# Optimization experiments

Hardware: AMD Instinct MI355X
Metric: run time of the kernel (lower is better)

## Reference

```python
import jax, jax.numpy as jnp
import numpy as np

H = W = 32      # latent grid
WS = 8          # window size
NH = 8          # heads
C = 512         # channels
SHIFTS = (0, WS // 2)  # depth-2 Swin stage: W-MSA then SW-MSA


def _rel_pos_index(ws):
    coords = np.stack(np.meshgrid(np.arange(ws), np.arange(ws), indexing='ij'))
    flat = coords.reshape(2, -1)
    rel = (flat[:, :, None] - flat[:, None, :]).transpose(1, 2, 0).copy()
    rel[:, :, 0] += ws - 1
    rel[:, :, 1] += ws - 1
    rel[:, :, 0] *= 2 * ws - 1
    return jnp.asarray(rel.sum(-1))  # (ws*ws, ws*ws) int


def _attn_mask(h, w, ws, shift):
    img = np.zeros((h, w))
    cnt = 0
    sl = (slice(0, -ws), slice(-ws, -shift), slice(-shift, None))
    for hs in sl:
        for wsl in sl:
            img[hs, wsl] = cnt
            cnt += 1
    mw = img.reshape(h // ws, ws, w // ws, ws).transpose(0, 2, 1, 3).reshape(-1, ws * ws)
    m = mw[:, None, :] - mw[:, :, None]  # matches unsqueeze(1) - unsqueeze(2)
    return jnp.asarray(np.where(m != 0, -100.0, 0.0).astype(np.float32))  # (nW, N, N)


def _ln(x, g, b, eps=1e-5):
    mu = x.mean(-1, keepdims=True)
    var = ((x - mu) ** 2).mean(-1, keepdims=True)
    return (x - mu) * jax.lax.rsqrt(var + eps) * g + b


def _swin_block(x, shift, mask, rpi, n1g, n1b, qw, qb, rpb, pw, pb, n2g, n2b, f1w, f1b, f2w, f2b):
    B, L, Cc = x.shape
    N = WS * WS
    hd = Cc // NH
    shortcut = x
    h = _ln(x, n1g, n1b).reshape(B, H, W, Cc)
    if shift > 0:
        h = jnp.roll(h, (-shift, -shift), (1, 2))
    # window partition -> (B*nW, N, C)
    hw = h.reshape(B, H // WS, WS, W // WS, WS, Cc).transpose(0, 1, 3, 2, 4, 5).reshape(-1, N, Cc)
    qkv = (hw @ qw + qb).reshape(-1, N, 3, NH, hd).transpose(2, 0, 3, 1, 4)
    q, k, v = qkv[0], qkv[1], qkv[2]
    attn = jnp.einsum('bhnd,bhmd->bhnm', q * (hd ** -0.5), k)
    bias = rpb[rpi.reshape(-1)].reshape(N, N, NH).transpose(2, 0, 1)  # (NH, N, N)
    attn = attn + bias[None]
    if mask is not None:
        nW = mask.shape[0]
        attn = attn.reshape(-1, nW, NH, N, N) + mask[None, :, None]
        attn = attn.reshape(-1, NH, N, N)
    attn = jax.nn.softmax(attn, axis=-1)
    o = jnp.einsum('bhnm,bhmd->bhnd', attn, v).transpose(0, 2, 1, 3).reshape(-1, N, Cc)
    o = o @ pw + pb
    # window reverse
    o = o.reshape(B, H // WS, W // WS, WS, WS, Cc).transpose(0, 1, 3, 2, 4, 5).reshape(B, H, W, Cc)
    if shift > 0:
        o = jnp.roll(o, (shift, shift), (1, 2))
    x = shortcut + o.reshape(B, L, Cc)
    h2 = _ln(x, n2g, n2b)
    x = x + (jax.nn.gelu(h2 @ f1w + f1b, approximate=False) @ f2w + f2b)
    return x


def setup_inputs() -> dict:
    key = jax.random.key(0)
    ks = jax.random.split(key, 8)
    B, D, K = 32, 2, 4096
    s = 0.02
    return {
        'x': jax.random.normal(ks[0], (B, H * W, C), jnp.float32),
        'norm1_g': jnp.ones((D, C), jnp.float32),
        'norm1_b': jnp.zeros((D, C), jnp.float32),
        'qkv_w': jax.random.normal(ks[1], (D, C, 3 * C), jnp.float32) * s,
        'qkv_b': jnp.zeros((D, 3 * C), jnp.float32),
        'rpb_table': jax.random.normal(ks[2], (D, (2 * WS - 1) ** 2, NH), jnp.float32) * s,
        'proj_w': jax.random.normal(ks[3], (D, C, C), jnp.float32) * s,
        'proj_b': jnp.zeros((D, C), jnp.float32),
        'norm2_g': jnp.ones((D, C), jnp.float32),
        'norm2_b': jnp.zeros((D, C), jnp.float32),
        'fc1_w': jax.random.normal(ks[4], (D, C, 4 * C), jnp.float32) * s,
        'fc1_b': jnp.zeros((D, 4 * C), jnp.float32),
        'fc2_w': jax.random.normal(ks[5], (D, 4 * C, C), jnp.float32) * s,
        'fc2_b': jnp.zeros((D, C), jnp.float32),
        'codebook': jax.random.normal(ks[6], (K, C), jnp.float32),
    }


def reference(x, norm1_g, norm1_b, qkv_w, qkv_b, rpb_table, proj_w, proj_b,
              norm2_g, norm2_b, fc1_w, fc1_b, fc2_w, fc2_b, codebook):
    B, L, Cc = x.shape
    rpi = _rel_pos_index(WS)
    masks = [None, _attn_mask(H, W, WS, SHIFTS[1])]
    for i, shift in enumerate(SHIFTS):
        x = _swin_block(x, shift, masks[i], rpi,
                        norm1_g[i], norm1_b[i], qkv_w[i], qkv_b[i], rpb_table[i],
                        proj_w[i], proj_b[i], norm2_g[i], norm2_b[i],
                        fc1_w[i], fc1_b[i], fc2_w[i], fc2_b[i])
    # nearest-neighbor codebook quantization (cdist + argmin + gather)
    flat = x.reshape(-1, Cc)
    d = ((flat ** 2).sum(-1, keepdims=True)
         - 2.0 * flat @ codebook.T
         + (codebook ** 2).sum(-1))  # (B*L, K)
    idx = jnp.argmin(d, axis=-1)
    quant = codebook[idx]
    # straight-through estimator
    quant = flat + jax.lax.stop_gradient(quant - flat)
    return quant.reshape(B, L, Cc), idx.reshape(B, L)
```

## Files before the change

kernel.cpp:

```cpp
#include <hip/hip_runtime.h>
#include <math.h>

#define DEV __device__ __forceinline__

typedef __attribute__((ext_vector_type(8))) _Float16 f16x8;
typedef __attribute__((ext_vector_type(8))) short short8;
typedef __attribute__((ext_vector_type(4))) float f32x4;

namespace {

constexpr int C = 512;
constexpr int ROWS = 32768;
constexpr float LSCALE = 2048.0f;
constexpr float LINV   = 1.0f / 2048.0f;
constexpr float F16MIN = 6.1035156e-5f;

DEV void f2hsplit(float x, short& hs, short& ls) {
  _Float16 h = (_Float16)x;
  float hf = (float)h;
  if (fabsf(hf) < F16MIN) { h = (_Float16)0.0f; hf = 0.f; }
  _Float16 l = (_Float16)((x - hf) * LSCALE);
  if (fabsf((float)l) < F16MIN) l = (_Float16)0.0f;
  hs = __builtin_bit_cast(short, h);
  ls = __builtin_bit_cast(short, l);
}

DEV unsigned umn(unsigned a, unsigned b) { return a < b ? a : b; }
DEV unsigned umx(unsigned a, unsigned b) { return a > b ? a : b; }

DEV unsigned packkey(float d, int col) {
  unsigned u = __builtin_bit_cast(unsigned, d);
  u = (u & 0x80000000u) ? ~u : (u | 0x80000000u);
  return (u & 0xFFFFF000u) | (unsigned)col;
}
DEV float unpackd(unsigned k) {
  unsigned u = (k & 0x80000000u) ? (k ^ 0x80000000u) : ~k;
  return __builtin_bit_cast(float, u);
}

DEV int rowmap(int r, int shift) {
  int b  = r >> 10;
  int w  = (r >> 6) & 15;
  int wy = w >> 2, wx = w & 3;
  int ii = r & 63;
  int iy = ii >> 3, ix = ii & 7;
  int y = (wy * 8 + iy + shift) & 31;
  int x = (wx * 8 + ix + shift) & 31;
  return (b << 10) + (y << 5) + x;
}

DEV int region(int y) { return (y < 24) ? 0 : ((y < 28) ? 1 : 2); }

typedef __attribute__((address_space(1))) const unsigned int gu32;
typedef __attribute__((address_space(3))) unsigned int lu32;
DEV void gload16(const void* g, void* l) {
  __builtin_amdgcn_global_load_lds((gu32*)g, (lu32*)l, 16, 0, 0);
}

__global__ __launch_bounds__(256) void ln_split_kernel(
    const float* __restrict__ src, short* __restrict__ Hp, short* __restrict__ Lp,
    const float* __restrict__ g, const float* __restrict__ b,
    int shift, int windowed) {
  int wid  = (blockIdx.x * 256 + threadIdx.x) >> 6;
  int lane = threadIdx.x & 63;
  if (wid >= ROWS) return;
  int srcRow = windowed ? rowmap(wid, shift) : wid;
  const float* s = src + (size_t)srcRow * C + lane * 8;
  float v[8];
  *(float4*)(v)     = *(const float4*)(s);
  *(float4*)(v + 4) = *(const float4*)(s + 4);
  float sum = 0.f;
#pragma unroll
  for (int j = 0; j < 8; j++) sum += v[j];
#pragma unroll
  for (int o = 32; o >= 1; o >>= 1) sum += __shfl_xor(sum, o);
  float mu = sum * (1.0f / 512.0f);
  float vs = 0.f;
#pragma unroll
  for (int j = 0; j < 8; j++) { float d = v[j] - mu; vs += d * d; }
#pragma unroll
  for (int o = 32; o >= 1; o >>= 1) vs += __shfl_xor(vs, o);
  float rs = rsqrtf(vs * (1.0f / 512.0f) + 1e-5f);
  float gg[8], bb[8];
  *(float4*)gg       = *(const float4*)&g[lane * 8];
  *(float4*)(gg + 4) = *(const float4*)&g[lane * 8 + 4];
  *(float4*)bb       = *(const float4*)&b[lane * 8];
  *(float4*)(bb + 4) = *(const float4*)&b[lane * 8 + 4];
  short8 hv, lv;
#pragma unroll
  for (int j = 0; j < 8; j++) {
    float o8 = (v[j] - mu) * rs * gg[j] + bb[j];
    short hh, ll;
    f2hsplit(o8, hh, ll);
    hv[j] = hh; lv[j] = ll;
  }
  *(short8*)&Hp[(size_t)wid * C + lane * 8] = hv;
  *(short8*)&Lp[(size_t)wid * C + lane * 8] = lv;
}

__global__ __launch_bounds__(256) void rowss_kernel(
    const float* __restrict__ src, float* __restrict__ dst, int nrows) {
  int wid  = (blockIdx.x * 256 + threadIdx.x) >> 6;
  int lane = threadIdx.x & 63;
  if (wid >= nrows) return;
  const float* s = src + (size_t)wid * C + lane * 8;
  float4 a  = *(const float4*)s;
  float4 b4 = *(const float4*)(s + 4);
  float sum = a.x*a.x + a.y*a.y + a.z*a.z + a.w*a.w
            + b4.x*b4.x + b4.y*b4.y + b4.z*b4.z + b4.w*b4.w;
#pragma unroll
  for (int o = 32; o >= 1; o >>= 1) sum += __shfl_xor(sum, o);
  if (lane == 0) dst[wid] = sum;
}

__global__ __launch_bounds__(256) void wconvT_kernel(
    const float* __restrict__ W, short* __restrict__ Hp, short* __restrict__ Lp,
    int K, int N) {
  __shared__ float t[32][33];
  int tx = threadIdx.x, ty = threadIdx.y;
  int n0 = blockIdx.x * 32, k0 = blockIdx.y * 32;
#pragma unroll
  for (int r = 0; r < 4; r++) {
    int k = ty + r * 8;
    t[k][tx] = W[(size_t)(k0 + k) * N + n0 + tx];
  }
  __syncthreads();
#pragma unroll
  for (int r = 0; r < 4; r++) {
    int n = ty + r * 8;
    short h, l;
    f2hsplit(t[tx][n], h, l);
    Hp[(size_t)(n0 + n) * K + k0 + tx] = h;
    Lp[(size_t)(n0 + n) * K + k0 + tx] = l;
  }
}

__global__ __launch_bounds__(256) void wconv_kernel(
    const float* __restrict__ W, short* __restrict__ Hp, short* __restrict__ Lp) {
  size_t i = ((size_t)blockIdx.x * 256 + threadIdx.x) * 4;
  float4 a = *(const float4*)&W[i];
  float v[4] = {a.x, a.y, a.z, a.w};
  short hv[4], lv[4];
#pragma unroll
  for (int j = 0; j < 4; j++) f2hsplit(v[j], hv[j], lv[j]);
  *(short4*)&Hp[i] = *(short4*)hv;
  *(short4*)&Lp[i] = *(short4*)lv;
}

template <int EPI>
__global__ __launch_bounds__(512) void mgemm(
    const short* __restrict__ Ah, const short* __restrict__ Al,
    const short* __restrict__ Bh, const short* __restrict__ Bl,
    const int K, const float* __restrict__ bias,
    float* __restrict__ outF, short* __restrict__ outH, short* __restrict__ outL,
    const int ldo,
    const float* __restrict__ resid, const int rowOff, const int perm, const int shift) {
  __shared__ short lds[32768];
  const int m0 = blockIdx.x * 128, n0 = blockIdx.y * 128;
  const int t  = threadIdx.x;
  const int wv = t >> 6, ln = t & 63;
  const int wr = (wv >> 2) * 64, wc = (wv & 3) * 32;
  const int l15 = ln & 15, l4 = ln >> 4;

  f32x4 accH[4][2], accL[4][2];
#pragma unroll
  for (int mf = 0; mf < 4; mf++)
#pragma unroll
    for (int nf = 0; nf < 2; nf++) {
      accH[mf][nf] = (f32x4){0.f, 0.f, 0.f, 0.f};
      accL[mf][nf] = (f32x4){0.f, 0.f, 0.f, 0.f};
    }

  const int srow = ln >> 2;
  const int scol = ((ln & 3) ^ ((ln >> 3) & 3)) * 8;

  auto stage = [&](int buf, int k0) {
    short* b = lds + buf * 16384;
    size_t ra = (size_t)(m0 + wv * 16 + srow) * K + k0 + scol;
    size_t rb = (size_t)(n0 + wv * 16 + srow) * K + k0 + scol;
    gload16(Ah + ra, b + wv * 512);
    gload16(Bh + rb, b + 4096 + wv * 512);
    gload16(Al + ra, b + 8192 + wv * 512);
    gload16(Bl + rb, b + 12288 + wv * 512);
  };
  auto frag = [&](const short* lt, int rbase) -> f16x8 {
    int r = rbase + l15;
    int kc = l4 ^ ((r >> 1) & 3);
    return *(const f16x8*)(lt + (r >> 4) * 512 + (r & 15) * 32 + kc * 8);
  };

  stage(0, 0);
  __syncthreads();
  int cur = 0;
  for (int k0 = 0; k0 < K; k0 += 32) {
    if (k0 + 32 < K) stage(cur ^ 1, k0 + 32);
    const short* base = lds + cur * 16384;
    const short* As_h = base;
    const short* Bs_h = base + 4096;
    const short* As_l = base + 8192;
    const short* Bs_l = base + 12288;
    f16x8 ah[4], bh[2], bl[2];
#pragma unroll
    for (int mf = 0; mf < 4; mf++) ah[mf] = frag(As_h, wr + mf * 16);
#pragma unroll
    for (int nf = 0; nf < 2; nf++) bh[nf] = frag(Bs_h, wc + nf * 16);
#pragma unroll
    for (int mf = 0; mf < 4; mf++)
#pragma unroll
      for (int nf = 0; nf < 2; nf++)
        accH[mf][nf] = __builtin_amdgcn_mfma_f32_16x16x32_f16(ah[mf], bh[nf], accH[mf][nf], 0, 0, 0);
#pragma unroll
    for (int nf = 0; nf < 2; nf++) bl[nf] = frag(Bs_l, wc + nf * 16);
#pragma unroll
    for (int mf = 0; mf < 4; mf++)
#pragma unroll
      for (int nf = 0; nf < 2; nf++)
        accL[mf][nf] = __builtin_amdgcn_mfma_f32_16x16x32_f16(ah[mf], bl[nf], accL[mf][nf], 0, 0, 0);
#pragma unroll
    for (int mf = 0; mf < 4; mf++) {
      f16x8 al = frag(As_l, wr + mf * 16);
#pragma unroll
      for (int nf = 0; nf < 2; nf++)
        accL[mf][nf] = __builtin_amdgcn_mfma_f32_16x16x32_f16(al, bh[nf], accL[mf][nf], 0, 0, 0);
    }
    __syncthreads();
    cur ^= 1;
  }

  f32x4 acc[4][2];
#pragma unroll
  for (int mf = 0; mf < 4; mf++)
#pragma unroll
    for (int nf = 0; nf < 2; nf++)
#pragma unroll
      for (int r = 0; r < 4; r++)
        acc[mf][nf][r] = fmaf(accL[mf][nf][r], LINV, accH[mf][nf][r]);

  if (EPI == 0) {
#pragma unroll
    for (int mf = 0; mf < 4; mf++)
#pragma unroll
      for (int r = 0; r < 4; r++) {
        int row = m0 + wr + mf * 16 + l4 * 4 + r;
        float* op = outF + (size_t)row * ldo;
#pragma unroll
        for (int nf = 0; nf < 2; nf++) {
          int col = n0 + wc + nf * 16 + l15;
          op[col] = acc[mf][nf][r] + bias[col];
        }
      }
  } else if (EPI == 1) {
#pragma unroll
    for (int mf = 0; mf < 4; mf++)
#pragma unroll
      for (int r = 0; r < 4; r++) {
        int row = m0 + wr + mf * 16 + l4 * 4 + r;
#pragma unroll
        for (int nf = 0; nf < 2; nf++) {
          int col = n0 + wc + nf * 16 + l15;
          float v = acc[mf][nf][r] + bias[col];
          v = 0.5f * v * (1.0f + erff(v * 0.70710678118654752f));
          short h, l;
          f2hsplit(v, h, l);
          outH[(size_t)row * ldo + col] = h;
          outL[(size_t)row * ldo + col] = l;
        }
      }
  } else {
#pragma unroll
    for (int mf = 0; mf < 4; mf++)
#pragma unroll
      for (int r = 0; r < 4; r++) {
        int row = m0 + wr + mf * 16 + l4 * 4 + r;
        int orow = perm ? rowmap(row, shift) : (row + rowOff);
        const float* rp = resid + (size_t)orow * ldo;
        float* op = outF + (size_t)orow * ldo;
#pragma unroll
        for (int nf = 0; nf < 2; nf++) {
          int col = n0 + wc + nf * 16 + l15;
          float v = rp[col] + acc[mf][nf][r] + bias[col];
          op[col] = v;
          if (EPI == 4) {
            short h, l;
            f2hsplit(v, h, l);
            outH[(size_t)orow * ldo + col] = h;
            outL[(size_t)orow * ldo + col] = l;
          }
        }
      }
  }
}

__global__ __launch_bounds__(512) void vqgemm(
    const short* __restrict__ Ah, const short* __restrict__ Bh,
    const float* __restrict__ c2, unsigned* __restrict__ pk) {
  __shared__ short lds[12288];
  const int bid = blockIdx.x;
  const int xcd = bid & 7, idx = bid >> 3;
  const int m0 = (xcd * 32 + (idx & 31)) * 128;
  const int ny = idx >> 5;
  const int n0 = ny * 256;
  const int K = 512;
  const int t  = threadIdx.x;
  const int wv = t >> 6, ln = t & 63;
  const int wr = (wv >> 2) * 64, wc = (wv & 3) * 64;
  const int l15 = ln & 15, l4 = ln >> 4;

  f32x4 acc[4][4];
#pragma unroll
  for (int mf = 0; mf < 4; mf++)
#pragma unroll
    for (int nf = 0; nf < 4; nf++) acc[mf][nf] = (f32x4){0.f, 0.f, 0.f, 0.f};

  const int srow = ln >> 2;
  const int scol = ((ln & 3) ^ ((ln >> 3) & 3)) * 8;

  short* As = lds;
  short* Bs = lds + 4096;

  auto frag = [&](const short* lt, int rbase) -> f16x8 {
    int r = rbase + l15;
    int kc = l4 ^ ((r >> 1) & 3);
    return *(const f16x8*)(lt + (r >> 4) * 512 + (r & 15) * 32 + kc * 8);
  };

  for (int k0 = 0; k0 < K; k0 += 32) {
#pragma unroll
    for (int q = 0; q < 3; q++) {
      int s = wv * 3 + q;
      int isA = (s < 8);
      int c = isA ? s : (s - 8);
      const short* src = isA ? Ah : Bh;
      short* dst = (isA ? As : Bs) + c * 512;
      int rowbase = (isA ? m0 : n0) + c * 16;
      size_t ga = (size_t)(rowbase + srow) * K + k0 + scol;
      gload16(src + ga, dst);
    }
    __syncthreads();
    f16x8 ah[4], bh[4];
#pragma unroll
    for (int mf = 0; mf < 4; mf++) ah[mf] = frag(As, wr + mf * 16);
#pragma unroll
    for (int nf = 0; nf < 4; nf++) bh[nf] = frag(Bs, wc + nf * 16);
#pragma unroll
    for (int mf = 0; mf < 4; mf++)
#pragma unroll
      for (int nf = 0; nf < 4; nf++)
        acc[mf][nf] = __builtin_amdgcn_mfma_f32_16x16x32_f16(ah[mf], bh[nf], acc[mf][nf], 0, 0, 0);
    __syncthreads();
  }

  unsigned* hk = (unsigned*)(void*)lds;
#pragma unroll
  for (int mf = 0; mf < 4; mf++)
#pragma unroll
    for (int r = 0; r < 4; r++) {
      int wrow = wr + mf * 16 + l4 * 4 + r;
      unsigned k1 = 0xFFFFFFFFu, k2 = 0xFFFFFFFFu;
#pragma unroll
      for (int nf = 0; nf < 4; nf++) {
        int col = n0 + wc + nf * 16 + l15;
        float d = c2[col] - 2.0f * acc[mf][nf][r];
        unsigned kk = packkey(d, col);
        if (kk < k1) { k2 = k1; k1 = kk; }
        else if (kk < k2) { k2 = kk; }
      }
#pragma unroll
      for (int o = 1; o <= 8; o <<= 1) {
        unsigned b1 = (unsigned)__shfl_xor((int)k1, o);
        unsigned b2 = (unsigned)__shfl_xor((int)k2, o);
        unsigned m1 = umn(k1, b1);
        unsigned m2 = umn(umx(k1, b1), umn(k2, b2));
        k1 = m1; k2 = m2;
      }
      if (l15 == 0) {
        hk[wrow * 8 + (wv & 3) * 2 + 0] = k1;
        hk[wrow * 8 + (wv & 3) * 2 + 1] = k2;
      }
    }
  __syncthreads();
  if (t < 128) {
    unsigned q1[4], q2[4];
#pragma unroll
    for (int i = 0; i < 4; i++) {
      q1[i] = hk[t * 8 + i * 2];
      q2[i] = hk[t * 8 + i * 2 + 1];
    }
    unsigned a1 = umn(q1[0], q1[1]);
    unsigned a2 = umn(umx(q1[0], q1[1]), umn(q2[0], q2[1]));
    unsigned b1 = umn(q1[2], q1[3]);
    unsigned b2 = umn(umx(q1[2], q1[3]), umn(q2[2], q2[3]));
    unsigned m1 = umn(a1, b1);
    unsigned m2 = umn(umx(a1, b1), umn(a2, b2));
    size_t base = (size_t)(m0 + t) * 32 + ny * 2;
    pk[base + 0] = m1;
    pk[base + 1] = m2;
  }
}

__global__ __launch_bounds__(256) void vq_out_kernel(
    const unsigned* __restrict__ pk, const float* __restrict__ x,
    const float* __restrict__ cb,
    float* __restrict__ outq, float* __restrict__ outidx) {
  int r = blockIdx.x * 4 + (threadIdx.x >> 6);
  int lane = threadIdx.x & 63;
  unsigned key = (lane < 32) ? pk[(size_t)r * 32 + lane] : 0xFFFFFFFFu;
  unsigned kmin = key;
#pragma unroll
  for (int o = 32; o >= 1; o >>= 1) kmin = umn(kmin, (unsigned)__shfl_xor((int)kmin, o));
  float dmin = unpackd(kmin);
  unsigned long long mask = __ballot(lane < 32 && unpackd(key) <= dmin + 2.0f);

  const float* xr = x + (size_t)r * C + lane * 8;
  float4 xa = *(const float4*)xr;
  float4 xb = *(const float4*)(xr + 4);

  float bestd = 3.4e38f;
  int   besti = 0x7fffffff;
  while (mask) {
    int l = __ffsll(mask) - 1;
    mask &= mask - 1;
    int col = ((unsigned)__shfl((int)key, l)) & 0xFFFu;
    const float* cr = cb + (size_t)col * C + lane * 8;
    float4 ca = *(const float4*)cr;
    float4 cb4 = *(const float4*)(cr + 4);
    float s = 0.f;
    s = fmaf(ca.x, ca.x - 2.f * xa.x, s);
    s = fmaf(ca.y, ca.y - 2.f * xa.y, s);
    s = fmaf(ca.z, ca.z - 2.f * xa.z, s);
    s = fmaf(ca.w, ca.w - 2.f * xa.w, s);
    s = fmaf(cb4.x, cb4.x - 2.f * xb.x, s);
    s = fmaf(cb4.y, cb4.y - 2.f * xb.y, s);
    s = fmaf(cb4.z, cb4.z - 2.f * xb.z, s);
    s = fmaf(cb4.w, cb4.w - 2.f * xb.w, s);
#pragma unroll
    for (int o = 32; o >= 1; o >>= 1) s += __shfl_xor(s, o);
    if (s < bestd || (s == bestd && col < besti)) { bestd = s; besti = col; }
  }
  const float4* src = (const float4*)(cb + (size_t)besti * C + lane * 8);
  float4*       dst = (float4*)(outq + (size_t)r * C + lane * 8);
  dst[0] = src[0];
  dst[1] = src[1];
  if (lane == 0) outidx[r] = (float)besti;
}

__global__ __launch_bounds__(256) void attn_kernel(
    const float* __restrict__ qkv,
    const float* __restrict__ rpb,
    short* __restrict__ Hout, short* __restrict__ Lout,
    int winOff, int shift) {
  int wl = blockIdx.x;
  int h  = blockIdx.y;
  int t  = threadIdx.x;
  __shared__ float q[64][64], k[64][64], v[64][64], pT[64][64];

  const float* base = qkv + (size_t)wl * 64 * 1536 + h * 64;
#pragma unroll
  for (int rep = 0; rep < 4; rep++) {
    int f = t + rep * 256;
    int i = f >> 4, dq = (f & 15) * 4;
    const float* rowp = base + (size_t)i * 1536 + dq;
    float4 qv = *(const float4*)(rowp);
    float4 kv = *(const float4*)(rowp + 512);
    float4 vv = *(const float4*)(rowp + 1024);
    q[i][dq] = qv.x * 0.125f; q[i][dq + 1] = qv.y * 0.125f;
    q[i][dq + 2] = qv.z * 0.125f; q[i][dq + 3] = qv.w * 0.125f;
    *(float4*)&k[i][dq] = kv;
    *(float4*)&v[i][dq] = vv;
  }
  __syncthreads();

  int i  = t >> 2;
  int jg = t & 3;
  int wim = (winOff + wl) & 15;
  int wy = wim >> 2, wx = wim & 3;
  int iy = i >> 3, ix = i & 7;

  float qreg[64];
#pragma unroll
  for (int d = 0; d < 64; d += 4) *(float4*)&qreg[d] = *(float4*)&q[i][d];

  int ci = 0;
  if (shift) ci = region(wy * 8 + iy) * 3 + region(wx * 8 + ix);

  float sc[16];
#pragma unroll
  for (int jj = 0; jj < 16; jj++) {
    int j = jg * 16 + jj;
    float s = 0.f;
#pragma unroll
    for (int d = 0; d < 64; d += 4) {
      float4 kv = *(float4*)&k[j][d];
      s = fmaf(qreg[d], kv.x, s);
      s = fmaf(qreg[d + 1], kv.y, s);
      s = fmaf(qreg[d + 2], kv.z, s);
      s = fmaf(qreg[d + 3], kv.w, s);
    }
    int jy = j >> 3, jx = j & 7;
    s += rpb[((iy - jy + 7) * 15 + (ix - jx + 7)) * 8 + h];
    if (shift) {
      int cj = region(wy * 8 + jy) * 3 + region(wx * 8 + jx);
      if (ci != cj) s -= 100.0f;
    }
    sc[jj] = s;
  }
  float mx = sc[0];
#pragma unroll
  for (int jj = 1; jj < 16; jj++) mx = fmaxf(mx, sc[jj]);
  mx = fmaxf(mx, __shfl_xor(mx, 1));
  mx = fmaxf(mx, __shfl_xor(mx, 2));
  float sum = 0.f;
#pragma unroll
  for (int jj = 0; jj < 16; jj++) { sc[jj] = expf(sc[jj] - mx); sum += sc[jj]; }
  sum += __shfl_xor(sum, 1);
  sum += __shfl_xor(sum, 2);
  float inv = 1.0f / sum;
#pragma unroll
  for (int jj = 0; jj < 16; jj++) pT[jg * 16 + jj][i] = sc[jj] * inv;
  __syncthreads();

  float accv[16];
#pragma unroll
  for (int dd = 0; dd < 16; dd++) accv[dd] = 0.f;
  for (int j = 0; j < 64; j++) {
    float pij = pT[j][i];
#pragma unroll
    for (int dd = 0; dd < 16; dd += 4) {
      float4 vv = *(float4*)&v[j][jg * 16 + dd];
      accv[dd]     = fmaf(pij, vv.x, accv[dd]);
      accv[dd + 1] = fmaf(pij, vv.y, accv[dd + 1]);
      accv[dd + 2] = fmaf(pij, vv.z, accv[dd + 2]);
      accv[dd + 3] = fmaf(pij, vv.w, accv[dd + 3]);
    }
  }
  size_t obase = ((size_t)(winOff + wl) * 64 + i) * 512 + h * 64 + jg * 16;
  short8 hv, lv;
#pragma unroll
  for (int half = 0; half < 2; half++) {
#pragma unroll
    for (int j = 0; j < 8; j++) {
      short hh, ll;
      f2hsplit(accv[half * 8 + j], hh, ll);
      hv[j] = hh; lv[j] = ll;
    }
    *(short8*)&Hout[obase + half * 8] = hv;
    *(short8*)&Lout[obase + half * 8] = lv;
  }
}

}

extern "C" void kernel_launch(void* const* d_in, const int* in_sizes, int n_in,
                              void* d_out, int out_size, void* d_ws, size_t ws_size,
                              hipStream_t stream) {
  const float* x_in = (const float*)d_in[0];
  const float* n1g  = (const float*)d_in[1];
  const float* n1b  = (const float*)d_in[2];
  const float* qkvw = (const float*)d_in[3];
  const float* qkvb = (const float*)d_in[4];
  const float* rpb  = (const float*)d_in[5];
  const float* pw   = (const float*)d_in[6];
  const float* pb   = (const float*)d_in[7];
  const float* n2g  = (const float*)d_in[8];
  const float* n2b  = (const float*)d_in[9];
  const float* f1w  = (const float*)d_in[10];
  const float* f1b  = (const float*)d_in[11];
  const float* f2w  = (const float*)d_in[12];
  const float* f2b_ = (const float*)d_in[13];
  const float* cb   = (const float*)d_in[14];

  float* outq   = (float*)d_out;
  float* outidx = outq + 16777216;
  short* Hbuf = (short*)d_out;
  short* Lbuf = Hbuf + (size_t)ROWS * 512;

  char* ws = (char*)d_ws;
  float* Abuf = (float*)ws;
  short* Wb   = (short*)(ws + ((size_t)64 << 20));
  char*  Cbuf = ws + ((size_t)96 << 20);
  const int Rrows = (ws_size >= ((size_t)232 << 20)) ? 16384
                  : (ws_size >= ((size_t)160 << 20)) ? 8192
                  : (ws_size >= ((size_t)128 << 20)) ? 4096 : 2048;

  const int SZ_QKV = 512 * 1536, SZ_P = 512 * 512, SZ_F1 = 512 * 2048, SZ_F2 = 2048 * 512;
  const int PB = (SZ_QKV + SZ_P + SZ_F1 + SZ_F2) * 2;
  short* cbH = Wb + (size_t)2 * PB;
  short* cbL = cbH + 4096 * 512;

  for (int blk = 0; blk < 2; blk++) {
    short* base = Wb + (size_t)blk * PB;
    short* qH = base;          short* qL = qH + SZ_QKV;
    short* pH = qL + SZ_QKV;   short* pL = pH + SZ_P;
    short* f1H = pL + SZ_P;    short* f1L = f1H + SZ_F1;
    short* f2H = f1L + SZ_F1;  short* f2L = f2H + SZ_F2;
    wconvT_kernel<<<dim3(48, 16), dim3(32, 8), 0, stream>>>(qkvw + (size_t)blk * SZ_QKV, qH, qL, 512, 1536);
    wconvT_kernel<<<dim3(16, 16), dim3(32, 8), 0, stream>>>(pw + (size_t)blk * SZ_P, pH, pL, 512, 512);
    wconvT_kernel<<<dim3(64, 16), dim3(32, 8), 0, stream>>>(f1w + (size_t)blk * SZ_F1, f1H, f1L, 512, 2048);
    wconvT_kernel<<<dim3(16, 64), dim3(32, 8), 0, stream>>>(f2w + (size_t)blk * SZ_F2, f2H, f2L, 2048, 512);
  }
  wconv_kernel<<<2048, 256, 0, stream>>>(cb, cbH, cbL);

  const int nch = ROWS / Rrows;
  for (int blk = 0; blk < 2; blk++) {
    short* base = Wb + (size_t)blk * PB;
    short* qH = base;          short* qL = qH + SZ_QKV;
    short* pH = qL + SZ_QKV;   short* pL = pH + SZ_P;
    short* f1H = pL + SZ_P;    short* f1L = f1H + SZ_F1;
    short* f2H = f1L + SZ_F1;  short* f2L = f2H + SZ_F2;
    const float* xcur = blk ? (const float*)Abuf : x_in;
    int shift = blk ? 4 : 0;

    ln_split_kernel<<<8192, 256, 0, stream>>>(xcur, Hbuf, Lbuf, n1g + blk * 512, n1b + blk * 512, shift, 1);

    float* Cq = (float*)Cbuf;
    for (int ch = 0; ch < nch; ch++) {
      int r0 = ch * Rrows;
      mgemm<0><<<dim3(Rrows / 128, 12), 512, 0, stream>>>(
          Hbuf + (size_t)r0 * 512, Lbuf + (size_t)r0 * 512, qH, qL, 512,
          qkvb + blk * 1536, Cq, nullptr, nullptr, 1536,
          nullptr, 0, 0, 0);
      attn_kernel<<<dim3(Rrows / 64, 8), 256, 0, stream>>>(
          Cq, rpb + blk * 1800, Hbuf, Lbuf, r0 >> 6, shift);
    }

    mgemm<2><<<dim3(256, 4), 512, 0, stream>>>(
        Hbuf, Lbuf, pH, pL, 512, pb + blk * 512,
        Abuf, nullptr, nullptr, 512,
        blk ? (const float*)Abuf : x_in, 0, 1, shift);

    ln_split_kernel<<<8192, 256, 0, stream>>>(Abuf, Hbuf, Lbuf, n2g + blk * 512, n2b + blk * 512, 0, 0);

    short* gh = (short*)Cbuf;
    short* gl = gh + (size_t)Rrows * 2048;
    for (int ch = 0; ch < nch; ch++) {
      int r0 = ch * Rrows;
      mgemm<1><<<dim3(Rrows / 128, 16), 512, 0, stream>>>(
          Hbuf + (size_t)r0 * 512, Lbuf + (size_t)r0 * 512, f1H, f1L, 512,
          f1b + blk * 2048, nullptr, gh, gl, 2048,
          nullptr, 0, 0, 0);
      if (blk == 0) {
        mgemm<2><<<dim3(Rrows / 128, 4), 512, 0, stream>>>(
            gh, gl, f2H, f2L, 2048, f2b_ + blk * 512,
            Abuf, nullptr, nullptr, 512,
            Abuf, r0, 0, 0);
      } else {
        mgemm<4><<<dim3(Rrows / 128, 4), 512, 0, stream>>>(
            gh, gl, f2H, f2L, 2048, f2b_ + blk * 512,
            Abuf, Hbuf, Lbuf, 512,
            Abuf, r0, 0, 0);
      }
    }
  }

  float*    c2  = (float*)Cbuf;
  unsigned* pkb = (unsigned*)(Cbuf + ((size_t)64 << 10));
  rowss_kernel<<<1024, 256, 0, stream>>>(cb, c2, 4096);
  vqgemm<<<4096, 512, 0, stream>>>(Hbuf, cbH, c2, pkb);
  vq_out_kernel<<<8192, 256, 0, stream>>>(pkb, Abuf, cb, outq, outidx);
}
```

Before: 2.331 ms.

## Widen split-fp16 GEMM tiles to 128x256 and double-buffer the VQ GEMM

Adds a wgemm kernel with 128x256 output tiles (16 accumulator fragments per wave for each of the high and low parts) and uses it for the QKV, attention projection and FC1 GEMMs, which halves the grid in N. This raises operand reuse per LDS load but roughly doubles accumulator registers and LDS (96KB), which may reduce occupancy. The VQ distance GEMM gains a double-buffered LDS staging pipeline so the next K-tile loads while the current one runs on MFMA. The mgemm kernel is trimmed to only its residual epilogues.

After: 2.724 ms. 16.8% more time.

```diff
diff --git a/kernel.cpp b/kernel.cpp
--- a/kernel.cpp
+++ b/kernel.cpp
@@ -145,6 +145,143 @@
   for (int j = 0; j < 4; j++) f2hsplit(v[j], hv[j], lv[j]);
   *(short4*)&Hp[i] = *(short4*)hv;
   *(short4*)&Lp[i] = *(short4*)lv;
+}
+
+template <int EPI>
+__global__ __launch_bounds__(512) void wgemm(
+    const short* __restrict__ Ah, const short* __restrict__ Al,
+    const short* __restrict__ Bh, const short* __restrict__ Bl,
+    const int K, const float* __restrict__ bias,
+    float* __restrict__ outF, short* __restrict__ outH, short* __restrict__ outL,
+    const int ldo,
+    const float* __restrict__ resid, const int rowOff, const int perm, const int shift) {
+  __shared__ short lds[49152];
+  const int m0 = blockIdx.x * 128, n0 = blockIdx.y * 256;
+  const int t  = threadIdx.x;
+  const int wv = t >> 6, ln = t & 63;
+  const int wr = (wv >> 2) * 64, wc = (wv & 3) * 64;
+  const int l15 = ln & 15, l4 = ln >> 4;
+
+  f32x4 accH[4][4], accL[4][4];
+#pragma unroll
+  for (int mf = 0; mf < 4; mf++)
+#pragma unroll
+    for (int nf = 0; nf < 4; nf++) {
+      accH[mf][nf] = (f32x4){0.f, 0.f, 0.f, 0.f};
+      accL[mf][nf] = (f32x4){0.f, 0.f, 0.f, 0.f};
+    }
+
+  const int srow = ln >> 2;
+  const int scol = ((ln & 3) ^ ((ln >> 3) & 3)) * 8;
+
+  auto stage = [&](int buf, int k0) {
+    short* b = lds + buf * 24576;
+#pragma unroll
+    for (int q = 0; q < 6; q++) {
+      int s = wv * 6 + q;
+      const short* src; short* dstp; int rowbase;
+      if (s < 8)       { src = Ah; dstp = b + s * 512;                rowbase = m0 + s * 16; }
+      else if (s < 24) { src = Bh; dstp = b + 4096 + (s - 8) * 512;   rowbase = n0 + (s - 8) * 16; }
+      else if (s < 32) { src = Al; dstp = b + 12288 + (s - 24) * 512; rowbase = m0 + (s - 24) * 16; }
+      else             { src = Bl; dstp = b + 16384 + (s - 32) * 512; rowbase = n0 + (s - 32) * 16; }
+      gload16(src + (size_t)(rowbase + srow) * K + k0 + scol, dstp);
+    }
+  };
+  auto frag = [&](const short* lt, int rbase) -> f16x8 {
+    int r = rbase + l15;
+    int kc = l4 ^ ((r >> 1) & 3);
+    return *(const f16x8*)(lt + (r >> 4) * 512 + (r & 15) * 32 + kc * 8);
+  };
+
+  stage(0, 0);
+  __syncthreads();
+  int cur = 0;
+  for (int k0 = 0; k0 < K; k0 += 32) {
+    if (k0 + 32 < K) stage(cur ^ 1, k0 + 32);
+    const short* b = lds + cur * 24576;
+    f16x8 ah[4], bh[4], bl[4];
+#pragma unroll
+    for (int mf = 0; mf < 4; mf++) ah[mf] = frag(b, wr + mf * 16);
+#pragma unroll
+    for (int nf = 0; nf < 4; nf++) bh[nf] = frag(b + 4096, wc + nf * 16);
+#pragma unroll
+    for (int mf = 0; mf < 4; mf++)
+#pragma unroll
+      for (int nf = 0; nf < 4; nf++)
+        accH[mf][nf] = __builtin_amdgcn_mfma_f32_16x16x32_f16(ah[mf], bh[nf], accH[mf][nf], 0, 0, 0);
+#pragma unroll
+    for (int nf = 0; nf < 4; nf++) bl[nf] = frag(b + 16384, wc + nf * 16);
+#pragma unroll
+    for (int mf = 0; mf < 4; mf++)
+#pragma unroll
+      for (int nf = 0; nf < 4; nf++)
+        accL[mf][nf] = __builtin_amdgcn_mfma_f32_16x16x32_f16(ah[mf], bl[nf], accL[mf][nf], 0, 0, 0);
+#pragma unroll
+    for (int mf = 0; mf < 4; mf++) {
+      f16x8 al = frag(b + 12288, wr + mf * 16);
+#pragma unroll
+      for (int nf = 0; nf < 4; nf++)
+        accL[mf][nf] = __builtin_amdgcn_mfma_f32_16x16x32_f16(al, bh[nf], accL[mf][nf], 0, 0, 0);
+    }
+    __syncthreads();
+    cur ^= 1;
+  }
+
+  f32x4 acc[4][4];
+#pragma unroll
+  for (int mf = 0; mf < 4; mf++)
+#pragma unroll
+    for (int nf = 0; nf < 4; nf++)
+#pragma unroll
+      for (int r = 0; r < 4; r++)
+        acc[mf][nf][r] = fmaf(accL[mf][nf][r], LINV, accH[mf][nf][r]);
+
+  if (EPI == 0) {
+#pragma unroll
+    for (int mf = 0; mf < 4; mf++)
+#pragma unroll
+      for (int r = 0; r < 4; r++) {
+        int row = m0 + wr + mf * 16 + l4 * 4 + r;
+        float* op = outF + (size_t)row * ldo;
+#pragma unroll
+        for (int nf = 0; nf < 4; nf++) {
+          int col = n0 + wc + nf * 16 + l15;
+          op[col] = acc[mf][nf][r] + bias[col];
+        }
+      }
+  } else if (EPI == 1) {
+#pragma unroll
+    for (int mf = 0; mf < 4; mf++)
+#pragma unroll
+      for (int r = 0; r < 4; r++) {
+        int row = m0 + wr + mf * 16 + l4 * 4 + r;
+#pragma unroll
+        for (int nf = 0; nf < 4; nf++) {
+          int col = n0 + wc + nf * 16 + l15;
+          float v = acc[mf][nf][r] + bias[col];
+          v = 0.5f * v * (1.0f + erff(v * 0.70710678118654752f));
+          short h, l;
+          f2hsplit(v, h, l);
+          outH[(size_t)row * ldo + col] = h;
+          outL[(size_t)row * ldo + col] = l;
+        }
+      }
+  } else {
+#pragma unroll
+    for (int mf = 0; mf < 4; mf++)
+#pragma unroll
+      for (int r = 0; r < 4; r++) {
+        int row = m0 + wr + mf * 16 + l4 * 4 + r;
+        int orow = perm ? rowmap(row, shift) : (row + rowOff);
+        const float* rp = resid + (size_t)orow * ldo;
+        float* op = outF + (size_t)orow * ldo;
+#pragma unroll
+        for (int nf = 0; nf < 4; nf++) {
+          int col = n0 + wc + nf * 16 + l15;
+          op[col] = rp[col] + acc[mf][nf][r] + bias[col];
+        }
+      }
+  }
 }
 
 template <int EPI>
@@ -195,22 +332,18 @@
   for (int k0 = 0; k0 < K; k0 += 32) {
     if (k0 + 32 < K) stage(cur ^ 1, k0 + 32);
     const short* base = lds + cur * 16384;
-    const short* As_h = base;
-    const short* Bs_h = base + 4096;
-    const short* As_l = base + 8192;
-    const short* Bs_l = base + 12288;
     f16x8 ah[4], bh[2], bl[2];
 #pragma unroll
-    for (int mf = 0; mf < 4; mf++) ah[mf] = frag(As_h, wr + mf * 16);
-#pragma unroll
-    for (int nf = 0; nf < 2; nf++) bh[nf] = frag(Bs_h, wc + nf * 16);
+    for (int mf = 0; mf < 4; mf++) ah[mf] = frag(base, wr + mf * 16);
+#pragma unroll
+    for (int nf = 0; nf < 2; nf++) bh[nf] = frag(base + 4096, wc + nf * 16);
 #pragma unroll
     for (int mf = 0; mf < 4; mf++)
 #pragma unroll
       for (int nf = 0; nf < 2; nf++)
         accH[mf][nf] = __builtin_amdgcn_mfma_f32_16x16x32_f16(ah[mf], bh[nf], accH[mf][nf], 0, 0, 0);
 #pragma unroll
-    for (int nf = 0; nf < 2; nf++) bl[nf] = frag(Bs_l, wc + nf * 16);
+    for (int nf = 0; nf < 2; nf++) bl[nf] = frag(base + 12288, wc + nf * 16);
 #pragma unroll
     for (int mf = 0; mf < 4; mf++)
 #pragma unroll
@@ -218,7 +351,7 @@
         accL[mf][nf] = __builtin_amdgcn_mfma_f32_16x16x32_f16(ah[mf], bl[nf], accL[mf][nf], 0, 0, 0);
 #pragma unroll
     for (int mf = 0; mf < 4; mf++) {
-      f16x8 al = frag(As_l, wr + mf * 16);
+      f16x8 al = frag(base + 8192, wr + mf * 16);
 #pragma unroll
       for (int nf = 0; nf < 2; nf++)
         accL[mf][nf] = __builtin_amdgcn_mfma_f32_16x16x32_f16(al, bh[nf], accL[mf][nf], 0, 0, 0);
@@ -236,37 +369,7 @@
       for (int r = 0; r < 4; r++)
         acc[mf][nf][r] = fmaf(accL[mf][nf][r], LINV, accH[mf][nf][r]);
 
-  if (EPI == 0) {
-#pragma unroll
-    for (int mf = 0; mf < 4; mf++)
-#pragma unroll
-      for (int r = 0; r < 4; r++) {
-        int row = m0 + wr + mf * 16 + l4 * 4 + r;
-        float* op = outF + (size_t)row * ldo;
-#pragma unroll
-        for (int nf = 0; nf < 2; nf++) {
-          int col = n0 + wc + nf * 16 + l15;
-          op[col] = acc[mf][nf][r] + bias[col];
-        }
-      }
-  } else if (EPI == 1) {
-#pragma unroll
-    for (int mf = 0; mf < 4; mf++)
-#pragma unroll
-      for (int r = 0; r < 4; r++) {
-        int row = m0 + wr + mf * 16 + l4 * 4 + r;
-#pragma unroll
-        for (int nf = 0; nf < 2; nf++) {
-          int col = n0 + wc + nf * 16 + l15;
-          float v = acc[mf][nf][r] + bias[col];
-          v = 0.5f * v * (1.0f + erff(v * 0.70710678118654752f));
-          short h, l;
-          f2hsplit(v, h, l);
-          outH[(size_t)row * ldo + col] = h;
-          outL[(size_t)row * ldo + col] = l;
-        }
-      }
-  } else {
+  {
 #pragma unroll
     for (int mf = 0; mf < 4; mf++)
 #pragma unroll
@@ -294,7 +397,7 @@
 __global__ __launch_bounds__(512) void vqgemm(
     const short* __restrict__ Ah, const short* __restrict__ Bh,
     const float* __restrict__ c2, unsigned* __restrict__ pk) {
-  __shared__ short lds[12288];
+  __shared__ short lds[24576];
   const int bid = blockIdx.x;
   const int xcd = bid & 7, idx = bid >> 3;
   const int m0 = (xcd * 32 + (idx & 31)) * 128;
@@ -315,39 +418,43 @@
   const int srow = ln >> 2;
   const int scol = ((ln & 3) ^ ((ln >> 3) & 3)) * 8;
 
-  short* As = lds;
-  short* Bs = lds + 4096;
-
+  auto stage = [&](int buf, int k0) {
+    short* b = lds + buf * 12288;
+#pragma unroll
+    for (int q = 0; q < 3; q++) {
+      int s = wv * 3 + q;
+      int isA = (s < 8);
+      int c = isA ? s : (s - 8);
+      const short* src = isA ? Ah : Bh;
+      short* dst = b + (isA ? c * 512 : 4096 + c * 512);
+      int rowbase = (isA ? m0 : n0) + c * 16;
+      gload16(src + (size_t)(rowbase + srow) * K + k0 + scol, dst);
+    }
+  };
   auto frag = [&](const short* lt, int rbase) -> f16x8 {
     int r = rbase + l15;
     int kc = l4 ^ ((r >> 1) & 3);
     return *(const f16x8*)(lt + (r >> 4) * 512 + (r & 15) * 32 + kc * 8);
   };
 
+  stage(0, 0);
+  __syncthreads();
+  int cur = 0;
   for (int k0 = 0; k0 < K; k0 += 32) {
-#pragma unroll
-    for (int q = 0; q < 3; q++) {
-      int s = wv * 3 + q;
-      int isA = (s < 8);
-      int c = isA ? s : (s - 8);
-      const short* src = isA ? Ah : Bh;
-      short* dst = (isA ? As : Bs) + c * 512;
-      int rowbase = (isA ? m0 : n0) + c * 16;
-      size_t ga = (size_t)(rowbase + srow) * K + k0 + scol;
-      gload16(src + ga, dst);
-    }
-    __syncthreads();
+    if (k0 + 32 < K) stage(cur ^ 1, k0 + 32);
+    const short* b = lds + cur * 12288;
     f16x8 ah[4], bh[4];
 #pragma unroll
-    for (int mf = 0; mf < 4; mf++) ah[mf] = frag(As, wr + mf * 16);
-#pragma unroll
-    for (int nf = 0; nf < 4; nf++) bh[nf] = frag(Bs, wc + nf * 16);
+    for (int mf = 0; mf < 4; mf++) ah[mf] = frag(b, wr + mf * 16);
+#pragma unroll
+    for (int nf = 0; nf < 4; nf++) bh[nf] = frag(b + 4096, wc + nf * 16);
 #pragma unroll
     for (int mf = 0; mf < 4; mf++)
 #pragma unroll
       for (int nf = 0; nf < 4; nf++)
         acc[mf][nf] = __builtin_amdgcn_mfma_f32_16x16x32_f16(ah[mf], bh[nf], acc[mf][nf], 0, 0, 0);
     __syncthreads();
+    cur ^= 1;
   }
 
   unsigned* hk = (unsigned*)(void*)lds;
@@ -615,7 +722,7 @@
     float* Cq = (float*)Cbuf;
     for (int ch = 0; ch < nch; ch++) {
       int r0 = ch * Rrows;
-      mgemm<0><<<dim3(Rrows / 128, 12), 512, 0, stream>>>(
+      wgemm<0><<<dim3(Rrows / 128, 6), 512, 0, stream>>>(
           Hbuf + (size_t)r0 * 512, Lbuf + (size_t)r0 * 512, qH, qL, 512,
           qkvb + blk * 1536, Cq, nullptr, nullptr, 1536,
           nullptr, 0, 0, 0);
@@ -623,7 +730,7 @@
           Cq, rpb + blk * 1800, Hbuf, Lbuf, r0 >> 6, shift);
     }
 
-    mgemm<2><<<dim3(256, 4), 512, 0, stream>>>(
+    wgemm<2><<<dim3(256, 2), 512, 0, stream>>>(
         Hbuf, Lbuf, pH, pL, 512, pb + blk * 512,
         Abuf, nullptr, nullptr, 512,
         blk ? (const float*)Abuf : x_in, 0, 1, shift);
@@ -634,7 +741,7 @@
     short* gl = gh + (size_t)Rrows * 2048;
     for (int ch = 0; ch < nch; ch++) {
       int r0 = ch * Rrows;
-      mgemm<1><<<dim3(Rrows / 128, 16), 512, 0, stream>>>(
+      wgemm<1><<<dim3(Rrows / 128, 8), 512, 0, stream>>>(
           Hbuf + (size_t)r0 * 512, Lbuf + (size_t)r0 * 512, f1H, f1L, 512,
           f1b + blk * 2048, nullptr, gh, gl, 2048,
           nullptr, 0, 0, 0);
```
